# Optimization experiments

Measured on AMD Instinct MI355X. Metric: run time of the kernel, lower is better.

Reference implementation:

```python
import jax, jax.numpy as jnp
import numpy as np

STRIDE = 16
H = 100
W = 100
C = 1024
A = 9  # anchors per location
IOU_THRESH = 0.7
MIN_SIZE = 16.0


def _conv2d(x, w, b):
    # x: [N,C,H,W], w: [O,I,kh,kw] (torch OIHW), 'same' padding, stride 1
    y = jax.lax.conv_general_dilated(
        x, w, window_strides=(1, 1), padding='SAME',
        dimension_numbers=('NCHW', 'OIHW', 'NCHW'))
    return y + b[None, :, None, None]


def _nms_keep(boxes, valid, iou_thresh):
    # boxes: [N,4] (y1,x1,y2,x2) sorted by descending score; valid: [N] bool
    n = boxes.shape[0]
    y1, x1, y2, x2 = boxes[:, 0], boxes[:, 1], boxes[:, 2], boxes[:, 3]
    areas = (y2 - y1) * (x2 - x1)
    idx = jnp.arange(n)

    def body(i, keep):
        iy1 = jnp.maximum(y1[i], y1)
        ix1 = jnp.maximum(x1[i], x1)
        iy2 = jnp.minimum(y2[i], y2)
        ix2 = jnp.minimum(x2[i], x2)
        inter = jnp.maximum(iy2 - iy1, 0.0) * jnp.maximum(ix2 - ix1, 0.0)
        iou = inter / (areas[i] + areas - inter + 1e-8)
        suppress = (iou > iou_thresh) & (idx > i)
        return jnp.where(keep[i], keep & ~suppress, keep)

    return jax.lax.fori_loop(0, n, body, valid)


def _make_anchor_map():
    ratios = np.array([0.5, 1.0, 2.0])
    sizes = np.array([128.0, 256.0, 512.0])
    ah = (sizes[:, None] * np.sqrt(ratios)[None, :]).reshape(-1)  # [9]
    aw = (sizes[:, None] / np.sqrt(ratios)[None, :]).reshape(-1)  # [9]
    cy = (np.arange(H) + 0.5) * STRIDE
    cx = (np.arange(W) + 0.5) * STRIDE
    am = np.zeros((H, W, A, 4), dtype=np.float32)
    am[..., 0] = cy[:, None, None]
    am[..., 1] = cx[None, :, None]
    am[..., 2] = ah[None, None, :]
    am[..., 3] = aw[None, None, :]
    return jnp.asarray(am.reshape(H, W, A * 4))


def setup_inputs() -> dict:
    key = jax.random.key(0)
    ks = jax.random.split(key, 4)
    feature_map = jax.random.normal(ks[0], (1, C, H, W), jnp.float32)
    # module init: normal(0, 0.01) weights, zero biases
    w1 = jax.random.normal(ks[1], (C, C, 3, 3), jnp.float32) * 0.01
    b1 = jnp.zeros((C,), jnp.float32)
    w_cls = jax.random.normal(ks[2], (A, C, 1, 1), jnp.float32) * 0.01
    b_cls = jnp.zeros((A,), jnp.float32)
    w_box = jax.random.normal(ks[3], (A * 4, C, 1, 1), jnp.float32) * 0.01
    b_box = jnp.zeros((A * 4,), jnp.float32)
    return {
        'feature_map': feature_map,
        'image_shape': jnp.array([3, H * STRIDE, W * STRIDE], jnp.int32),
        'anchor_map': _make_anchor_map(),
        'anchor_valid_map': jnp.ones((H, W, A), jnp.int32),
        'max_proposals_pre_nms': 6000,
        'max_proposals_post_nms': 300,
        'w1': w1, 'b1': b1,
        'w_cls': w_cls, 'b_cls': b_cls,
        'w_box': w_box, 'b_box': b_box,
    }


def reference(feature_map, image_shape, anchor_map, anchor_valid_map,
              max_proposals_pre_nms, max_proposals_post_nms,
              w1, b1, w_cls, b_cls, w_box, b_box):
    pre = int(max_proposals_pre_nms)
    post = int(max_proposals_post_nms)

    y = jax.nn.relu(_conv2d(feature_map, w1, b1))
    objectness_score_map = jax.nn.sigmoid(_conv2d(y, w_cls, b_cls))  # [1,9,H,W]
    box_deltas_map = _conv2d(y, w_box, b_box)                        # [1,36,H,W]
    # NCHW -> NHWC, like permute(0,2,3,1)
    objectness_score_map = jnp.transpose(objectness_score_map, (0, 2, 3, 1))
    box_deltas_map = jnp.transpose(box_deltas_map, (0, 2, 3, 1))

    h, w, a = anchor_valid_map.shape
    n = h * w * a
    anchors = anchor_map.reshape(n, 4)                # (cy, cx, ah, aw)
    scores = objectness_score_map.reshape(n)
    deltas = jax.lax.stop_gradient(box_deltas_map.reshape(n, 4))  # .detach()
    # allow_edge_proposals=True -> no valid filtering

    # decode (means=0, stds=1): center = c + t*s, size = s*exp(t)
    center = anchors[:, 0:2] + deltas[:, 0:2] * anchors[:, 2:4]
    size = anchors[:, 2:4] * jnp.exp(deltas[:, 2:4])
    proposals = jnp.concatenate([center - 0.5 * size, center + 0.5 * size], axis=1)

    # argsort ascending then flip == descending (matches torch code)
    order = jnp.argsort(scores)[::-1][:pre]
    proposals = proposals[order]
    scores_sorted = scores[order]

    # clip to image
    y1x1 = jnp.maximum(proposals[:, 0:2], 0.0)
    y2 = jnp.minimum(proposals[:, 2], image_shape[1].astype(proposals.dtype))
    x2 = jnp.minimum(proposals[:, 3], image_shape[2].astype(proposals.dtype))
    proposals = jnp.concatenate([y1x1, y2[:, None], x2[:, None]], axis=1)

    height = proposals[:, 2] - proposals[:, 0]
    width = proposals[:, 3] - proposals[:, 1]
    valid = (height >= MIN_SIZE) & (width >= MIN_SIZE)

    keep = _nms_keep(proposals, valid, IOU_THRESH)

    # fixed-shape selection of first `post` kept boxes (score-ordered)
    pos = jnp.where(keep, jnp.arange(pre), pre)
    pos = jnp.sort(pos)[:post]
    ok = pos < pre
    safe = jnp.minimum(pos, pre - 1)
    out_proposals = jnp.where(ok[:, None], proposals[safe], 0.0)  # [post,4]

    return objectness_score_map, box_deltas_map, out_proposals
```

## Files before the change

kernel.cpp:

```cpp
#include <hip/hip_runtime.h>
#include <hip/hip_fp16.h>
#include <stdint.h>

#define HH 100
#define WW 100
#define NPIX 10000
#define CIN 1024
#define COUT 1024
#define NA 9
#define NANCH 90000
#define PRE 6000
#define POST 300
#define SORTN 131072
#define MASKW 96
#define NW 94
#define K9 9216
#define SPAD 10404
#define WSCALE 1024.0f
#define KH 48

#define PXT 160
#define ABYTES 8192
#define BBYTES 10240
#define BUFB 36864
#define NSTEP 288

typedef unsigned short u16;
typedef _Float16 f16x8 __attribute__((ext_vector_type(8)));
typedef float f32x4 __attribute__((ext_vector_type(4)));

__device__ __forceinline__ void gload16(const u16* g, char* l)
{
    __builtin_amdgcn_global_load_lds((const void*)g, (void*)l, 16, 0, 0);
}

__global__ __launch_bounds__(256) void xsplit(
    const float* __restrict__ x, u16* __restrict__ xt1, u16* __restrict__ xt2)
{
    __shared__ unsigned sh[32][257];
    const int t = threadIdx.x;
    const int px0 = blockIdx.x * 32;
    const int ci0 = blockIdx.y * 256;
    for (int it = 0; it < 32; ++it) {
        int idx = it * 256 + t;
        int a = idx >> 5, b = idx & 31;
        int p = px0 + b;
        float v = (p < NPIX) ? x[(size_t)(ci0 + a) * NPIX + p] : 0.f;
        __half h1 = __float2half_rn(v);
        __half h2 = __float2half_rn(v - __half2float(h1));
        sh[b][a] = ((unsigned)__half_as_ushort(h1) << 16) | __half_as_ushort(h2);
    }
    __syncthreads();
    for (int it = 0; it < 8; ++it) {
        int u = it * 256 + t;
        int pl = u >> 6, cq = u & 63;
        int p = px0 + pl;
        if (p >= NPIX) continue;
        int r = p / 100, c = p - r * 100;
        int spx = (r + 1) * 102 + (c + 1);
        unsigned w0 = sh[pl][cq * 4 + 0], w1 = sh[pl][cq * 4 + 1];
        unsigned w2 = sh[pl][cq * 4 + 2], w3 = sh[pl][cq * 4 + 3];
        ushort4 v1 = make_ushort4((u16)(w0 >> 16), (u16)(w1 >> 16), (u16)(w2 >> 16), (u16)(w3 >> 16));
        ushort4 v2 = make_ushort4((u16)(w0 & 0xffff), (u16)(w1 & 0xffff), (u16)(w2 & 0xffff), (u16)(w3 & 0xffff));
        size_t o = (size_t)spx * 1024 + ci0 + cq * 4;
        *(ushort4*)&xt1[o] = v1;
        *(ushort4*)&xt2[o] = v2;
    }
}

__global__ __launch_bounds__(256) void xborder(u16* __restrict__ xt1, u16* __restrict__ xt2)
{
    const int idx = blockIdx.x;
    int spx;
    if (idx < 102) spx = idx;
    else if (idx < 204) spx = 10302 + (idx - 102);
    else { int k = idx - 204; spx = (1 + (k >> 1)) * 102 + (k & 1) * 101; }
    const int t = threadIdx.x;
    size_t o = (size_t)spx * 1024 + t * 4;
    *(ushort4*)&xt1[o] = make_ushort4(0, 0, 0, 0);
    *(ushort4*)&xt2[o] = make_ushort4(0, 0, 0, 0);
}

__global__ __launch_bounds__(256) void wsplit(
    const float* __restrict__ w1, u16* __restrict__ wp1, u16* __restrict__ wp2)
{
    __shared__ float sw[K9];
    const int t = threadIdx.x;
    const int co = blockIdx.x;
    for (int it = 0; it < 36; ++it)
        sw[it * 256 + t] = w1[(size_t)co * K9 + it * 256 + t];
    __syncthreads();
    for (int tap = 0; tap < 9; ++tap) {
        for (int it = 0; it < 4; ++it) {
            int ci = it * 256 + t;
            float v = sw[ci * 9 + tap] * WSCALE;
            __half h1 = __float2half_rn(v);
            __half h2 = __float2half_rn(v - __half2float(h1));
            size_t o = (size_t)tap * (COUT * 1024) + (size_t)co * 1024 + ci;
            wp1[o] = __half_as_ushort(h1);
            wp2[o] = __half_as_ushort(h2);
        }
    }
}

__global__ __launch_bounds__(256, 2) void conv_mfma(
    const u16* __restrict__ xt1, const u16* __restrict__ xt2,
    const u16* __restrict__ wp1, const u16* __restrict__ wp2,
    const float* __restrict__ b1, float* __restrict__ y)
{
    __shared__ __align__(16) char lds[2 * BUFB];
    const int t = threadIdx.x;
    const int co0 = blockIdx.x * 128;
    const int px0 = blockIdx.y * PXT;
    const int lane = t & 63;
    const int wv = __builtin_amdgcn_readfirstlane(t >> 6);
    const int wm = (wv >> 1) * 64;
    const int wn = (wv & 1) * 80;

    const int qs = (lane & 3) ^ ((lane >> 3) & 3);
    const int aln = (lane >> 2) * 1024 + qs * 8;

    const int ar0 = wv * 32, ar1 = wv * 32 + 16;
    const size_t aOff0 = (size_t)(co0 + ar0) * 1024 + aln;
    const size_t aOff1 = (size_t)(co0 + ar1) * 1024 + aln;

    const int nb = (wv < 2) ? 3 : 2;
    size_t bOff[3]; int bLds[3];
#pragma unroll
    for (int s = 0; s < 3; ++s) {
        int r0 = (wv + 4 * s) * 16;
        if (r0 >= PXT) r0 = 0;
        int p = px0 + r0 + (lane >> 2);
        if (p > NPIX - 1) p = NPIX - 1;
        int rr = p / 100, cc = p - rr * 100;
        bOff[s] = (size_t)((rr + 1) * 102 + cc + 1) * 1024 + qs * 8;
        bLds[s] = r0 * 64;
    }

    const int qf = ((lane >> 4) ^ (((lane & 15) >> 1) & 3)) * 16;
    const int fA = (wm + (lane & 15)) * 64 + qf;
    const int fB = 16384 + (wn + (lane & 15)) * 64 + qf;

    f32x4 acc[4][5] = {};

    auto STAGE = [&](int buf, int tap, int ci0) {
        const int dy = (tap * 11) >> 5;
        const int tsh = (dy - 1) * 102 + (tap - dy * 3) - 1;
        const size_t adelta = (size_t)tap * 1048576 + ci0;
        const ptrdiff_t bdelta = (ptrdiff_t)tsh * 1024 + ci0;
        char* lb = lds + buf * BUFB;
        gload16(wp1 + aOff0 + adelta, lb + ar0 * 64);
        gload16(wp1 + aOff1 + adelta, lb + ar1 * 64);
        gload16(wp2 + aOff0 + adelta, lb + ABYTES + ar0 * 64);
        gload16(wp2 + aOff1 + adelta, lb + ABYTES + ar1 * 64);
#pragma unroll
        for (int s = 0; s < 3; ++s) {
            if (s < nb) {
                gload16(xt1 + (ptrdiff_t)bOff[s] + bdelta, lb + 16384 + bLds[s]);
                gload16(xt2 + (ptrdiff_t)bOff[s] + bdelta, lb + 26624 + bLds[s]);
            }
        }
    };

    auto COMPUTE = [&](int buf) {
        const char* lb = lds + buf * BUFB;
        f16x8 A1[4], A2[4], B1[5], B2[5];
#pragma unroll
        for (int mi = 0; mi < 4; ++mi) {
            A1[mi] = *(const f16x8*)(lb + fA + mi * 1024);
            A2[mi] = *(const f16x8*)(lb + ABYTES + fA + mi * 1024);
        }
#pragma unroll
        for (int ni = 0; ni < 5; ++ni) {
            B1[ni] = *(const f16x8*)(lb + fB + ni * 1024);
            B2[ni] = *(const f16x8*)(lb + BBYTES + fB + ni * 1024);
        }
#pragma unroll
        for (int mi = 0; mi < 4; ++mi)
#pragma unroll
            for (int ni = 0; ni < 5; ++ni) {
                acc[mi][ni] = __builtin_amdgcn_mfma_f32_16x16x32_f16(A1[mi], B1[ni], acc[mi][ni], 0, 0, 0);
                acc[mi][ni] = __builtin_amdgcn_mfma_f32_16x16x32_f16(A1[mi], B2[ni], acc[mi][ni], 0, 0, 0);
                acc[mi][ni] = __builtin_amdgcn_mfma_f32_16x16x32_f16(A2[mi], B1[ni], acc[mi][ni], 0, 0, 0);
            }
    };

    STAGE(0, 0, 0);
    __syncthreads();
    for (int kk = 0; kk < NSTEP - 1; ++kk) {
        const int kn = kk + 1;
        STAGE(kn & 1, kn >> 5, (kn & 31) << 5);
        COMPUTE(kk & 1);
        __syncthreads();
    }
    COMPUTE((NSTEP - 1) & 1);

    const int q4 = (lane >> 4) * 4, nl = lane & 15;
    const float inv = 1.0f / WSCALE;
#pragma unroll
    for (int mi = 0; mi < 4; ++mi) {
        const int cob = co0 + wm + mi * 16 + q4;
        const float bb0 = b1[cob + 0], bb1 = b1[cob + 1];
        const float bb2 = b1[cob + 2], bb3 = b1[cob + 3];
#pragma unroll
        for (int ni = 0; ni < 5; ++ni) {
            const int px = px0 + wn + ni * 16 + nl;
            if (px < NPIX) {
                y[(size_t)(cob + 0) * NPIX + px] = fmaxf(acc[mi][ni][0] * inv + bb0, 0.f);
                y[(size_t)(cob + 1) * NPIX + px] = fmaxf(acc[mi][ni][1] * inv + bb1, 0.f);
                y[(size_t)(cob + 2) * NPIX + px] = fmaxf(acc[mi][ni][2] * inv + bb2, 0.f);
                y[(size_t)(cob + 3) * NPIX + px] = fmaxf(acc[mi][ni][3] * inv + bb3, 0.f);
            }
        }
    }
}

__global__ __launch_bounds__(256) void wh_prep(
    const float* __restrict__ wcls, const float* __restrict__ wbox,
    float* __restrict__ wh)
{
    int e = blockIdx.x * 256 + threadIdx.x;
    if (e >= CIN * KH) return;
    int c = e / KH, k = e - c * KH;
    float v = 0.f;
    if (k < 9) v = wcls[k * CIN + c];
    else if (k < 45) v = wbox[(k - 9) * CIN + c];
    wh[e] = v;
}

__global__ __launch_bounds__(256) void rpn_head(
    const float* __restrict__ y, const float* __restrict__ wh,
    const float* __restrict__ bcls, const float* __restrict__ bbox,
    const float* __restrict__ am, const int* __restrict__ ishape,
    float* __restrict__ out_scores, float* __restrict__ out_deltas,
    float4* __restrict__ boxes, unsigned long long* __restrict__ keys)
{
    __shared__ float red[4][64][KH + 1];
    const int t = threadIdx.x;
    const int lane = t & 63;
    const int q = __builtin_amdgcn_readfirstlane(t >> 6);
    const int p = blockIdx.x * 64 + lane;
    const int pp = (p < NPIX) ? p : (NPIX - 1);

    float acc[45];
#pragma unroll
    for (int k = 0; k < 45; ++k) acc[k] = 0.f;

    const float* __restrict__ yq  = y  + (size_t)q * 256 * NPIX + pp;
    const float* __restrict__ whq = wh + (size_t)q * 256 * KH;
    for (int c = 0; c < 256; ++c) {
        float yv = yq[(size_t)c * NPIX];
        const float* wr = whq + c * KH;
#pragma unroll
        for (int k = 0; k < 45; ++k) acc[k] += yv * wr[k];
    }

#pragma unroll
    for (int k = 0; k < 45; ++k) red[q][lane][k] = acc[k];
    __syncthreads();

    if (t >= 64 || p >= NPIX) return;

    float s[45];
#pragma unroll
    for (int k = 0; k < 45; ++k)
        s[k] = (red[0][lane][k] + red[1][lane][k]) + (red[2][lane][k] + red[3][lane][k]);

    const float imh = (float)ishape[1], imw = (float)ishape[2];
#pragma unroll
    for (int a = 0; a < 9; ++a) {
        const int i = p * NA + a;
        float logit = s[a] + bcls[a];
        float score = 1.f / (1.f + expf(-logit));
        float d0 = s[9 + a * 4 + 0] + bbox[a * 4 + 0];
        float d1 = s[9 + a * 4 + 1] + bbox[a * 4 + 1];
        float d2 = s[9 + a * 4 + 2] + bbox[a * 4 + 2];
        float d3 = s[9 + a * 4 + 3] + bbox[a * 4 + 3];
        out_scores[i] = score;
        out_deltas[i * 4 + 0] = d0;
        out_deltas[i * 4 + 1] = d1;
        out_deltas[i * 4 + 2] = d2;
        out_deltas[i * 4 + 3] = d3;

        float cy = am[i * 4 + 0], cx = am[i * 4 + 1];
        float ah = am[i * 4 + 2], aw = am[i * 4 + 3];
        float ctry = cy + d0 * ah, ctrx = cx + d1 * aw;
        float hh = ah * expf(d2), ww = aw * expf(d3);
        float y1 = fmaxf(ctry - 0.5f * hh, 0.f);
        float x1 = fmaxf(ctrx - 0.5f * ww, 0.f);
        float y2 = fminf(ctry + 0.5f * hh, imh);
        float x2 = fminf(ctrx + 0.5f * ww, imw);
        boxes[i] = make_float4(y1, x1, y2, x2);
        unsigned sb = __float_as_uint(score);
        keys[i] = ((unsigned long long)sb << 32) | (unsigned)i;
    }
}

__global__ __launch_bounds__(256) void key_pad(unsigned long long* __restrict__ keys)
{
    int i = NANCH + blockIdx.x * 256 + threadIdx.x;
    if (i < SORTN) keys[i] = 0ull;
}

__global__ __launch_bounds__(256) void bitonic_local(unsigned long long* keys)
{
    __shared__ unsigned long long s[2048];
    const int base = blockIdx.x * 2048, t = threadIdx.x;
    for (int k = t; k < 2048; k += 256) s[k] = keys[base + k];
    for (int L = 2; L <= 2048; L <<= 1) {
        for (int d = L >> 1; d >= 1; d >>= 1) {
            __syncthreads();
            for (int pr = t; pr < 1024; pr += 256) {
                int i = ((pr & ~(d - 1)) << 1) | (pr & (d - 1));
                int j = i + d;
                bool desc = (((base + i) & L) == 0);
                unsigned long long va = s[i], vb = s[j];
                bool sw = desc ? (va < vb) : (va > vb);
                if (sw) { s[i] = vb; s[j] = va; }
            }
        }
    }
    __syncthreads();
    for (int k = t; k < 2048; k += 256) keys[base + k] = s[k];
}

__global__ __launch_bounds__(256) void bitonic_gpass(unsigned long long* keys, int L, int d)
{
    int pr = blockIdx.x * 256 + threadIdx.x;
    int i = ((pr & ~(d - 1)) << 1) | (pr & (d - 1));
    int j = i + d;
    bool desc = ((i & L) == 0);
    unsigned long long va = keys[i], vb = keys[j];
    bool sw = desc ? (va < vb) : (va > vb);
    if (sw) { keys[i] = vb; keys[j] = va; }
}

__global__ __launch_bounds__(256) void bitonic_lmerge(unsigned long long* keys, int L)
{
    __shared__ unsigned long long s[2048];
    const int base = blockIdx.x * 2048, t = threadIdx.x;
    for (int k = t; k < 2048; k += 256) s[k] = keys[base + k];
    const bool desc = ((base & L) == 0);
    for (int d = 1024; d >= 1; d >>= 1) {
        __syncthreads();
        for (int pr = t; pr < 1024; pr += 256) {
            int i = ((pr & ~(d - 1)) << 1) | (pr & (d - 1));
            int j = i + d;
            unsigned long long va = s[i], vb = s[j];
            bool sw = desc ? (va < vb) : (va > vb);
            if (sw) { s[i] = vb; s[j] = va; }
        }
    }
    __syncthreads();
    for (int k = t; k < 2048; k += 256) keys[base + k] = s[k];
}

__global__ __launch_bounds__(256) void gather_sorted(
    const unsigned long long* __restrict__ keys, const float4* __restrict__ boxes,
    float4* __restrict__ box_s, unsigned long long* __restrict__ validw)
{
    int s = blockIdx.x * 256 + threadIdx.x;
    bool valid = false;
    if (s < PRE) {
        unsigned idx = (unsigned)(keys[s] & 0xffffffffull);
        float4 b = boxes[idx];
        box_s[s] = b;
        valid = ((b.z - b.x) >= 16.f) && ((b.w - b.y) >= 16.f);
    }
    unsigned long long bal = __ballot(valid);
    if ((threadIdx.x & 63) == 0) validw[s >> 6] = bal;
}

__global__ __launch_bounds__(128) void nms_mask(
    const float4* __restrict__ box_s, unsigned long long* __restrict__ mask)
{
    const int i = blockIdx.x;
    const int w = threadIdx.x;
    if (w >= NW) return;
    float4 bi = box_s[i];
    float areai = (bi.z - bi.x) * (bi.w - bi.y);
    unsigned long long m = 0ull;
    const int j0 = w * 64;
    if (j0 + 63 > i) {
#pragma unroll 4
        for (int b = 0; b < 64; ++b) {
            int j = j0 + b;
            if (j <= i || j >= PRE) continue;
            float4 bj = box_s[j];
            float areaj = (bj.z - bj.x) * (bj.w - bj.y);
            float iy1 = fmaxf(bi.x, bj.x), ix1 = fmaxf(bi.y, bj.y);
            float iy2 = fminf(bi.z, bj.z), ix2 = fminf(bi.w, bj.w);
            float inter = fmaxf(iy2 - iy1, 0.f) * fmaxf(ix2 - ix1, 0.f);
            float iou = inter / (areai + areaj - inter + 1e-8f);
            if (iou > 0.7f) m |= (1ull << b);
        }
    }
    mask[(size_t)i * MASKW + w] = m;
}

__global__ __launch_bounds__(64) void nms_scan(
    const unsigned long long* __restrict__ mask,
    const unsigned long long* __restrict__ validw,
    unsigned long long* __restrict__ keepw)
{
    const int l = threadIdx.x;
    unsigned long long r0 = ~validw[l];
    unsigned long long r1 = (l < NW - 64) ? ~validw[64 + l] : ~0ull;

    unsigned long long p0[16], p1[16];
#pragma unroll
    for (int k = 0; k < 16; ++k) {
        p0[k] = mask[(size_t)k * MASKW + l];
        p1[k] = (l < NW - 64) ? mask[(size_t)k * MASKW + 64 + l] : 0ull;
    }
    int kept = 0;
    for (int w = 0; w < NW && kept < POST; ++w) {
        unsigned long long Wc = (w < 64) ? __shfl(r0, w) : __shfl(r1, w - 64);
#pragma unroll 16
        for (int b = 0; b < 64; ++b) {
            int i = w * 64 + b;
            if (i >= PRE) break;
            int slot = i & 15;
            unsigned long long m0 = p0[slot], m1 = p1[slot];
            int nxt = i + 16;
            if (nxt < PRE) {
                p0[slot] = mask[(size_t)nxt * MASKW + l];
                p1[slot] = (l < NW - 64) ? mask[(size_t)nxt * MASKW + 64 + l] : 0ull;
            }
            if (!((Wc >> b) & 1ull)) {
                r0 |= m0; r1 |= m1;
                Wc = (w < 64) ? __shfl(r0, w) : __shfl(r1, w - 64);
                ++kept;
            }
        }
    }
    keepw[l] = ~r0;
    if (l < NW - 64) keepw[64 + l] = ~r1;
}

__global__ __launch_bounds__(256) void out_gather(
    const unsigned long long* __restrict__ keepw,
    const float4* __restrict__ box_s, float* __restrict__ outp)
{
    __shared__ unsigned long long kw_s[NW];
    __shared__ int prefix[NW];
    const int t = threadIdx.x;
    if (t < NW) kw_s[t] = keepw[t];
    __syncthreads();
    if (t == 0) {
        int cum = 0;
        for (int w = 0; w < NW; ++w) { prefix[w] = cum; cum += __popcll(kw_s[w]); }
    }
    for (int k = t; k < POST * 4; k += 256) outp[k] = 0.f;
    __syncthreads();
    for (int i = t; i < PRE; i += 256) {
        int w = i >> 6, b = i & 63;
        unsigned long long kw = kw_s[w];
        if ((kw >> b) & 1ull) {
            int rank = prefix[w] + __popcll(kw & ((1ull << b) - 1ull));
            if (rank < POST) {
                float4 bx = box_s[i];
                outp[rank * 4 + 0] = bx.x;
                outp[rank * 4 + 1] = bx.y;
                outp[rank * 4 + 2] = bx.z;
                outp[rank * 4 + 3] = bx.w;
            }
        }
    }
}

extern "C" void kernel_launch(void* const* d_in, const int* in_sizes, int n_in,
                              void* d_out, int out_size, void* d_ws, size_t ws_size,
                              hipStream_t stream)
{
    const float* x      = (const float*)d_in[0];
    const int*   ishape = (const int*)  d_in[1];
    const float* am     = (const float*)d_in[2];
    const float* w1   = (const float*)d_in[6];
    const float* b1   = (const float*)d_in[7];
    const float* wcls = (const float*)d_in[8];
    const float* bcls = (const float*)d_in[9];
    const float* wbox = (const float*)d_in[10];
    const float* bbox = (const float*)d_in[11];
    float* out = (float*)d_out;

    char* ws = (char*)d_ws;
    size_t off = 0;
    float* y  = (float*)(ws + off);  off += (size_t)COUT * NPIX * 4;
    u16* xt1  = (u16*)(ws + off);    off += (size_t)SPAD * 1024 * 2;
    u16* xt2  = (u16*)(ws + off);    off += (size_t)SPAD * 1024 * 2;
    u16* wp1  = (u16*)(ws + off);    off += (size_t)9 * COUT * 1024 * 2;
    u16* wp2  = (u16*)(ws + off);    off += (size_t)9 * COUT * 1024 * 2;
    float4* boxes = (float4*)(ws + off);              off += (size_t)NANCH * 16;
    unsigned long long* keys = (unsigned long long*)(ws + off); off += (size_t)SORTN * 8;
    float4* box_s = (float4*)(ws + off);              off += (size_t)PRE * 16;
    unsigned long long* validw = (unsigned long long*)(ws + off); off += 96 * 8;
    unsigned long long* keepw  = (unsigned long long*)(ws + off); off += 96 * 8;
    unsigned long long* maskb  = (unsigned long long*)(ws + off); off += (size_t)PRE * MASKW * 8;
    float* wh = (float*)(ws + off);  off += (size_t)CIN * KH * 4;

    xsplit<<<dim3(313, 4), 256, 0, stream>>>(x, xt1, xt2);
    xborder<<<404, 256, 0, stream>>>(xt1, xt2);
    wsplit<<<COUT, 256, 0, stream>>>(w1, wp1, wp2);
    wh_prep<<<(CIN * KH + 255) / 256, 256, 0, stream>>>(wcls, wbox, wh);
    conv_mfma<<<dim3(8, (NPIX + PXT - 1) / PXT), 256, 0, stream>>>(xt1, xt2, wp1, wp2, b1, y);
    rpn_head<<<(NPIX + 63) / 64, 256, 0, stream>>>(y, wh, bcls, bbox, am, ishape,
                                                   out, out + NANCH, boxes, keys);
    key_pad<<<(SORTN - NANCH + 255) / 256, 256, 0, stream>>>(keys);
    bitonic_local<<<SORTN / 2048, 256, 0, stream>>>(keys);
    for (int L = 4096; L <= SORTN; L <<= 1) {
        for (int d = L >> 1; d >= 2048; d >>= 1)
            bitonic_gpass<<<SORTN / 512, 256, 0, stream>>>(keys, L, d);
        bitonic_lmerge<<<SORTN / 2048, 256, 0, stream>>>(keys, L);
    }
    gather_sorted<<<24, 256, 0, stream>>>(keys, boxes, box_s, validw);
    nms_mask<<<PRE, 128, 0, stream>>>(box_s, maskb);
    nms_scan<<<1, 64, 0, stream>>>(maskb, validw, keepw);
    out_gather<<<1, 256, 0, stream>>>(keepw, box_s, out + (size_t)NANCH * 5);
}
```

Measured before the change: 1.138 ms.

## Merge small prep/sort/NMS kernels and enlarge bitonic shared-memory tiles to 8K

Folds xborder into xsplit, wh_prep into wsplit, key_pad into rpn_head, gather_sorted into the final bitonic merge, and nms_scan plus out_gather into a single kernel, by giving the merged kernels extra blocks or extra tail work. It also grows the bitonic local sort and merge tiles from 2048 to 8192 keys with 1024-thread blocks, which cuts the number of global passes. The goal is to remove launch overhead and global round-trips in the post-conv pipeline. The cost is lower occupancy from 64KB of shared memory per block and only 16 blocks for the sort stages.

```diff
diff --git a/kernel.cpp b/kernel.cpp
--- a/kernel.cpp
+++ b/kernel.cpp
@@ -25,6 +25,8 @@
 #define BUFB 36864
 #define NSTEP 288
 
+#define HEADB 157
+
 typedef unsigned short u16;
 typedef _Float16 f16x8 __attribute__((ext_vector_type(8)));
 typedef float f32x4 __attribute__((ext_vector_type(4)));
@@ -39,6 +41,17 @@
 {
     __shared__ unsigned sh[32][257];
     const int t = threadIdx.x;
+    if (blockIdx.x >= 313) {
+        int idx = (blockIdx.x - 313) * 4 + blockIdx.y;
+        int spx;
+        if (idx < 102) spx = idx;
+        else if (idx < 204) spx = 10302 + (idx - 102);
+        else { int k = idx - 204; spx = (1 + (k >> 1)) * 102 + (k & 1) * 101; }
+        size_t o = (size_t)spx * 1024 + t * 4;
+        *(ushort4*)&xt1[o] = make_ushort4(0, 0, 0, 0);
+        *(ushort4*)&xt2[o] = make_ushort4(0, 0, 0, 0);
+        return;
+    }
     const int px0 = blockIdx.x * 32;
     const int ci0 = blockIdx.y * 256;
     for (int it = 0; it < 32; ++it) {
@@ -68,24 +81,24 @@
     }
 }
 
-__global__ __launch_bounds__(256) void xborder(u16* __restrict__ xt1, u16* __restrict__ xt2)
-{
-    const int idx = blockIdx.x;
-    int spx;
-    if (idx < 102) spx = idx;
-    else if (idx < 204) spx = 10302 + (idx - 102);
-    else { int k = idx - 204; spx = (1 + (k >> 1)) * 102 + (k & 1) * 101; }
-    const int t = threadIdx.x;
-    size_t o = (size_t)spx * 1024 + t * 4;
-    *(ushort4*)&xt1[o] = make_ushort4(0, 0, 0, 0);
-    *(ushort4*)&xt2[o] = make_ushort4(0, 0, 0, 0);
-}
-
 __global__ __launch_bounds__(256) void wsplit(
-    const float* __restrict__ w1, u16* __restrict__ wp1, u16* __restrict__ wp2)
+    const float* __restrict__ w1, u16* __restrict__ wp1, u16* __restrict__ wp2,
+    const float* __restrict__ wcls, const float* __restrict__ wbox,
+    float* __restrict__ wh)
 {
     __shared__ float sw[K9];
     const int t = threadIdx.x;
+    if (blockIdx.x >= COUT) {
+        int e = (blockIdx.x - COUT) * 256 + t;
+        if (e < CIN * KH) {
+            int c = e / KH, k = e - c * KH;
+            float v = 0.f;
+            if (k < 9) v = wcls[k * CIN + c];
+            else if (k < 45) v = wbox[(k - 9) * CIN + c];
+            wh[e] = v;
+        }
+        return;
+    }
     const int co = blockIdx.x;
     for (int it = 0; it < 36; ++it)
         sw[it * 256 + t] = w1[(size_t)co * K9 + it * 256 + t];
@@ -215,19 +228,6 @@
     }
 }
 
-__global__ __launch_bounds__(256) void wh_prep(
-    const float* __restrict__ wcls, const float* __restrict__ wbox,
-    float* __restrict__ wh)
-{
-    int e = blockIdx.x * 256 + threadIdx.x;
-    if (e >= CIN * KH) return;
-    int c = e / KH, k = e - c * KH;
-    float v = 0.f;
-    if (k < 9) v = wcls[k * CIN + c];
-    else if (k < 45) v = wbox[(k - 9) * CIN + c];
-    wh[e] = v;
-}
-
 __global__ __launch_bounds__(256) void rpn_head(
     const float* __restrict__ y, const float* __restrict__ wh,
     const float* __restrict__ bcls, const float* __restrict__ bbox,
@@ -237,6 +237,11 @@
 {
     __shared__ float red[4][64][KH + 1];
     const int t = threadIdx.x;
+    if (blockIdx.x >= HEADB) {
+        int i = NANCH + (blockIdx.x - HEADB) * 256 + t;
+        if (i < SORTN) keys[i] = 0ull;
+        return;
+    }
     const int lane = t & 63;
     const int q = __builtin_amdgcn_readfirstlane(t >> 6);
     const int p = blockIdx.x * 64 + lane;
@@ -296,21 +301,15 @@
     }
 }
 
-__global__ __launch_bounds__(256) void key_pad(unsigned long long* __restrict__ keys)
-{
-    int i = NANCH + blockIdx.x * 256 + threadIdx.x;
-    if (i < SORTN) keys[i] = 0ull;
-}
-
-__global__ __launch_bounds__(256) void bitonic_local(unsigned long long* keys)
-{
-    __shared__ unsigned long long s[2048];
-    const int base = blockIdx.x * 2048, t = threadIdx.x;
-    for (int k = t; k < 2048; k += 256) s[k] = keys[base + k];
-    for (int L = 2; L <= 2048; L <<= 1) {
+__global__ __launch_bounds__(1024) void bitonic_local8k(unsigned long long* keys)
+{
+    __shared__ unsigned long long s[8192];
+    const int base = blockIdx.x * 8192, t = threadIdx.x;
+    for (int k = t; k < 8192; k += 1024) s[k] = keys[base + k];
+    for (int L = 2; L <= 8192; L <<= 1) {
         for (int d = L >> 1; d >= 1; d >>= 1) {
             __syncthreads();
-            for (int pr = t; pr < 1024; pr += 256) {
+            for (int pr = t; pr < 4096; pr += 1024) {
                 int i = ((pr & ~(d - 1)) << 1) | (pr & (d - 1));
                 int j = i + d;
                 bool desc = (((base + i) & L) == 0);
@@ -321,7 +320,7 @@
         }
     }
     __syncthreads();
-    for (int k = t; k < 2048; k += 256) keys[base + k] = s[k];
+    for (int k = t; k < 8192; k += 1024) keys[base + k] = s[k];
 }
 
 __global__ __launch_bounds__(256) void bitonic_gpass(unsigned long long* keys, int L, int d)
@@ -335,15 +334,18 @@
     if (sw) { keys[i] = vb; keys[j] = va; }
 }
 
-__global__ __launch_bounds__(256) void bitonic_lmerge(unsigned long long* keys, int L)
-{
-    __shared__ unsigned long long s[2048];
-    const int base = blockIdx.x * 2048, t = threadIdx.x;
-    for (int k = t; k < 2048; k += 256) s[k] = keys[base + k];
+__global__ __launch_bounds__(1024) void bitonic_lmerge8k(
+    unsigned long long* keys, int L,
+    const float4* __restrict__ boxes, float4* __restrict__ box_s,
+    unsigned long long* __restrict__ validw)
+{
+    __shared__ unsigned long long s[8192];
+    const int base = blockIdx.x * 8192, t = threadIdx.x;
+    for (int k = t; k < 8192; k += 1024) s[k] = keys[base + k];
     const bool desc = ((base & L) == 0);
-    for (int d = 1024; d >= 1; d >>= 1) {
+    for (int d = 4096; d >= 1; d >>= 1) {
         __syncthreads();
-        for (int pr = t; pr < 1024; pr += 256) {
+        for (int pr = t; pr < 4096; pr += 1024) {
             int i = ((pr & ~(d - 1)) << 1) | (pr & (d - 1));
             int j = i + d;
             unsigned long long va = s[i], vb = s[j];
@@ -352,23 +354,20 @@
         }
     }
     __syncthreads();
-    for (int k = t; k < 2048; k += 256) keys[base + k] = s[k];
-}
-
-__global__ __launch_bounds__(256) void gather_sorted(
-    const unsigned long long* __restrict__ keys, const float4* __restrict__ boxes,
-    float4* __restrict__ box_s, unsigned long long* __restrict__ validw)
-{
-    int s = blockIdx.x * 256 + threadIdx.x;
-    bool valid = false;
-    if (s < PRE) {
-        unsigned idx = (unsigned)(keys[s] & 0xffffffffull);
-        float4 b = boxes[idx];
-        box_s[s] = b;
-        valid = ((b.z - b.x) >= 16.f) && ((b.w - b.y) >= 16.f);
-    }
-    unsigned long long bal = __ballot(valid);
-    if ((threadIdx.x & 63) == 0) validw[s >> 6] = bal;
+    for (int k = t; k < 8192; k += 1024) keys[base + k] = s[k];
+    if (L == SORTN && blockIdx.x == 0) {
+        for (int k = t; k < 6144; k += 1024) {
+            bool valid = false;
+            if (k < PRE) {
+                unsigned idx = (unsigned)(s[k] & 0xffffffffull);
+                float4 b = boxes[idx];
+                box_s[k] = b;
+                valid = ((b.z - b.x) >= 16.f) && ((b.w - b.y) >= 16.f);
+            }
+            unsigned long long bal = __ballot(valid);
+            if ((t & 63) == 0) validw[k >> 6] = bal;
+        }
+    }
 }
 
 __global__ __launch_bounds__(128) void nms_mask(
@@ -398,54 +397,48 @@
     mask[(size_t)i * MASKW + w] = m;
 }
 
-__global__ __launch_bounds__(64) void nms_scan(
+__global__ __launch_bounds__(256) void nms_scan_out(
     const unsigned long long* __restrict__ mask,
     const unsigned long long* __restrict__ validw,
-    unsigned long long* __restrict__ keepw)
-{
-    const int l = threadIdx.x;
-    unsigned long long r0 = ~validw[l];
-    unsigned long long r1 = (l < NW - 64) ? ~validw[64 + l] : ~0ull;
-
-    unsigned long long p0[16], p1[16];
-#pragma unroll
-    for (int k = 0; k < 16; ++k) {
-        p0[k] = mask[(size_t)k * MASKW + l];
-        p1[k] = (l < NW - 64) ? mask[(size_t)k * MASKW + 64 + l] : 0ull;
-    }
-    int kept = 0;
-    for (int w = 0; w < NW && kept < POST; ++w) {
-        unsigned long long Wc = (w < 64) ? __shfl(r0, w) : __shfl(r1, w - 64);
-#pragma unroll 16
-        for (int b = 0; b < 64; ++b) {
-            int i = w * 64 + b;
-            if (i >= PRE) break;
-            int slot = i & 15;
-            unsigned long long m0 = p0[slot], m1 = p1[slot];
-            int nxt = i + 16;
-            if (nxt < PRE) {
-                p0[slot] = mask[(size_t)nxt * MASKW + l];
-                p1[slot] = (l < NW - 64) ? mask[(size_t)nxt * MASKW + 64 + l] : 0ull;
-            }
-            if (!((Wc >> b) & 1ull)) {
-                r0 |= m0; r1 |= m1;
-                Wc = (w < 64) ? __shfl(r0, w) : __shfl(r1, w - 64);
-                ++kept;
-            }
-        }
-    }
-    keepw[l] = ~r0;
-    if (l < NW - 64) keepw[64 + l] = ~r1;
-}
-
-__global__ __launch_bounds__(256) void out_gather(
-    const unsigned long long* __restrict__ keepw,
     const float4* __restrict__ box_s, float* __restrict__ outp)
 {
     __shared__ unsigned long long kw_s[NW];
     __shared__ int prefix[NW];
     const int t = threadIdx.x;
-    if (t < NW) kw_s[t] = keepw[t];
+    if (t < 64) {
+        const int l = t;
+        unsigned long long r0 = ~validw[l];
+        unsigned long long r1 = (l < NW - 64) ? ~validw[64 + l] : ~0ull;
+        unsigned long long p0[16], p1[16];
+#pragma unroll
+        for (int k = 0; k < 16; ++k) {
+            p0[k] = mask[(size_t)k * MASKW + l];
+            p1[k] = (l < NW - 64) ? mask[(size_t)k * MASKW + 64 + l] : 0ull;
+        }
+        int kept = 0;
+        for (int w = 0; w < NW && kept < POST; ++w) {
+            unsigned long long Wc = (w < 64) ? __shfl(r0, w) : __shfl(r1, w - 64);
+#pragma unroll 16
+            for (int b = 0; b < 64; ++b) {
+                int i = w * 64 + b;
+                if (i >= PRE) break;
+                int slot = i & 15;
+                unsigned long long m0 = p0[slot], m1 = p1[slot];
+                int nxt = i + 16;
+                if (nxt < PRE) {
+                    p0[slot] = mask[(size_t)nxt * MASKW + l];
+                    p1[slot] = (l < NW - 64) ? mask[(size_t)nxt * MASKW + 64 + l] : 0ull;
+                }
+                if (!((Wc >> b) & 1ull)) {
+                    r0 |= m0; r1 |= m1;
+                    Wc = (w < 64) ? __shfl(r0, w) : __shfl(r1, w - 64);
+                    ++kept;
+                }
+            }
+        }
+        kw_s[l] = ~r0;
+        if (l < NW - 64) kw_s[64 + l] = ~r1;
+    }
     __syncthreads();
     if (t == 0) {
         int cum = 0;
@@ -495,26 +488,20 @@
     unsigned long long* keys = (unsigned long long*)(ws + off); off += (size_t)SORTN * 8;
     float4* box_s = (float4*)(ws + off);              off += (size_t)PRE * 16;
     unsigned long long* validw = (unsigned long long*)(ws + off); off += 96 * 8;
-    unsigned long long* keepw  = (unsigned long long*)(ws + off); off += 96 * 8;
     unsigned long long* maskb  = (unsigned long long*)(ws + off); off += (size_t)PRE * MASKW * 8;
     float* wh = (float*)(ws + off);  off += (size_t)CIN * KH * 4;
 
-    xsplit<<<dim3(313, 4), 256, 0, stream>>>(x, xt1, xt2);
-    xborder<<<404, 256, 0, stream>>>(xt1, xt2);
-    wsplit<<<COUT, 256, 0, stream>>>(w1, wp1, wp2);
-    wh_prep<<<(CIN * KH + 255) / 256, 256, 0, stream>>>(wcls, wbox, wh);
+    xsplit<<<dim3(414, 4), 256, 0, stream>>>(x, xt1, xt2);
+    wsplit<<<COUT + (CIN * KH + 255) / 256, 256, 0, stream>>>(w1, wp1, wp2, wcls, wbox, wh);
     conv_mfma<<<dim3(8, (NPIX + PXT - 1) / PXT), 256, 0, stream>>>(xt1, xt2, wp1, wp2, b1, y);
-    rpn_head<<<(NPIX + 63) / 64, 256, 0, stream>>>(y, wh, bcls, bbox, am, ishape,
-                                                   out, out + NANCH, boxes, keys);
-    key_pad<<<(SORTN - NANCH + 255) / 256, 256, 0, stream>>>(keys);
-    bitonic_local<<<SORTN / 2048, 256, 0, stream>>>(keys);
-    for (int L = 4096; L <= SORTN; L <<= 1) {
-        for (int d = L >> 1; d >= 2048; d >>= 1)
+    rpn_head<<<HEADB + (SORTN - NANCH + 255) / 256, 256, 0, stream>>>(
+        y, wh, bcls, bbox, am, ishape, out, out + NANCH, boxes, keys);
+    bitonic_local8k<<<SORTN / 8192, 1024, 0, stream>>>(keys);
+    for (int L = 16384; L <= SORTN; L <<= 1) {
+        for (int d = L >> 1; d >= 8192; d >>= 1)
             bitonic_gpass<<<SORTN / 512, 256, 0, stream>>>(keys, L, d);
-        bitonic_lmerge<<<SORTN / 2048, 256, 0, stream>>>(keys, L);
-    }
-    gather_sorted<<<24, 256, 0, stream>>>(keys, boxes, box_s, validw);
+        bitonic_lmerge8k<<<SORTN / 8192, 1024, 0, stream>>>(keys, L, boxes, box_s, validw);
+    }
     nms_mask<<<PRE, 128, 0, stream>>>(box_s, maskb);
-    nms_scan<<<1, 64, 0, stream>>>(maskb, validw, keepw);
-    out_gather<<<1, 256, 0, stream>>>(keepw, box_s, out + (size_t)NANCH * 5);
-}
+    nms_scan_out<<<1, 256, 0, stream>>>(maskb, validw, box_s, out + (size_t)NANCH * 5);
+}
```

Result: no change. 1.148 ms (+0.9%).
